# Optimization experiments

Hardware: AMD Instinct MI355X
Metric: run time of the kernel (lower is better)

## Reference

```python
import jax, jax.numpy as jnp
import numpy as np

EPS = 0.001  # additive floor applied after relu, as in the torch code


def setup_inputs() -> dict:
    key = jax.random.key(0)
    kA, kB, kW = jax.random.split(key, 3)
    M, N, C, H, W = 512, 64, 128, 8, 8
    A = jax.random.normal(kA, (M, C, H, W), dtype=jnp.float32)
    B = jax.random.normal(kB, (N, C, H, W), dtype=jnp.float32)
    Wg = jax.random.normal(kW, (C, C), dtype=jnp.float32) * 0.01  # Wg.data.normal_(0.0, 0.01)
    return {"A": A, "B": B, "Wg": Wg}


def reference(A, B, Wg):
    # Faithful vectorization of MIMOcom.get_source_dst_max(A, B, dir=True).
    # Torch loops i,j over HxW: B0 = B[:, i, j, :]; G = B0 @ Wg;
    # combination[m, n, p] = sum_c A[m, p, c] * G[n, c]; running max over (i, j).
    M, C, H, W = A.shape
    N = B.shape[0]
    P = H * W
    Af = jnp.transpose(A, (0, 2, 3, 1)).reshape(M, P, C)  # [M, P, C]
    Bf = jnp.transpose(B, (0, 2, 3, 1)).reshape(N, P, C)  # [N, Q, C]
    G = Bf @ Wg                                           # [N, Q, D]
    scores = jnp.einsum('mpd,nqd->mnpq', Af, G)           # [M, N, P, Q]
    comb_max = scores.max(axis=-1)                        # max over B positions q
    return jax.nn.relu(comb_max) + EPS                    # [M, N, P]
```

## Files before the change

kernel.cpp:

```cpp
#include <hip/hip_runtime.h>
#include <hip/hip_bf16.h>
#include <stdint.h>

typedef __attribute__((ext_vector_type(8))) short bf16x8;
typedef __attribute__((ext_vector_type(16))) float f32x16;
using bf16 = __hip_bfloat16;

static constexpr int Mdim = 512;
static constexpr int Ndim = 64;
static constexpr int Cdim = 128;
static constexpr int Pdim = 64;
static constexpr float EPS_ADD = 0.001f;

#define SB0 __builtin_amdgcn_sched_barrier(0)
#define WAITV(N) asm volatile("s_waitcnt vmcnt(" #N ")" ::: "memory")

__device__ __forceinline__ void gll16(const void* gsrc, void* ldst) {
    const __attribute__((address_space(1))) unsigned int* g =
        (const __attribute__((address_space(1))) unsigned int*)gsrc;
    __attribute__((address_space(3))) unsigned int* l =
        (__attribute__((address_space(3))) unsigned int*)(uintptr_t)ldst;
    __builtin_amdgcn_global_load_lds(g, l, 16, 0, 0);
}

__global__ void prep_kernel(const float* __restrict__ A, const float* __restrict__ B,
                            const float* __restrict__ Wg,
                            bf16* __restrict__ Afrag, bf16* __restrict__ Gfrag) {
    __shared__ float lds[128 * 65];
    const int t = threadIdx.x;

    if (blockIdx.x < 512) {
        const int m = blockIdx.x;
        const float* __restrict__ Am = A + (size_t)m * (Cdim * Pdim);
#pragma unroll
        for (int i = 0; i < 8; ++i) {
            int v = t + i * 256;
            int gidx = v * 4;
            int c = gidx >> 6, p = gidx & 63;
            float4 val = *reinterpret_cast<const float4*>(Am + gidx);
            float* dst = &lds[c * 65 + p];
            dst[0] = val.x; dst[1] = val.y; dst[2] = val.z; dst[3] = val.w;
        }
        __syncthreads();

        unsigned* __restrict__ dst32 = (unsigned*)(Afrag + (size_t)m * 8192);
#pragma unroll
        for (int i = 0; i < 16; ++i) {
            int pr = t + i * 256;
            int p = pr >> 6;
            int c = (pr & 63) << 1;
            float f0 = lds[c * 65 + p];
            float f1 = lds[(c + 1) * 65 + p];
            union { bf16 hh[2]; unsigned u; } pk;
            pk.hh[0] = __float2bfloat16(f0);
            pk.hh[1] = __float2bfloat16(f1);
            int h = p >> 5, l31 = p & 31;
            int ks = c >> 4, hi = (c >> 3) & 1, e = c & 7;
            dst32[h * 2048 + ks * 256 + hi * 128 + l31 * 4 + (e >> 1)] = pk.u;
        }
    } else {
        const int nb = blockIdx.x - 512;
        const int n  = nb >> 2;
        const int q0 = (nb & 3) * 16;
        const float* __restrict__ Bn = B + (size_t)n * (Cdim * Pdim);
#pragma unroll
        for (int i = 0; i < 8; ++i) {
            int v = t + i * 256;
            int gidx = v * 4;
            int c = gidx >> 6, q = gidx & 63;
            float4 val = *reinterpret_cast<const float4*>(Bn + gidx);
            float* dst = &lds[c * 65 + q];
            dst[0] = val.x; dst[1] = val.y; dst[2] = val.z; dst[3] = val.w;
        }
        __syncthreads();

        const int d  = t & 127;
        const int qb = q0 + (t >> 7) * 8;
        float acc[8] = {0.f, 0.f, 0.f, 0.f, 0.f, 0.f, 0.f, 0.f};
        for (int c = 0; c < 128; ++c) {
            float w = Wg[c * 128 + d];
#pragma unroll
            for (int qi = 0; qi < 8; ++qi)
                acc[qi] = fmaf(lds[c * 65 + qb + qi], w, acc[qi]);
        }
        bf16* __restrict__ gdst = Gfrag + (size_t)n * 8192;
        const int ks = d >> 4, hi = (d >> 3) & 1, e = d & 7;
#pragma unroll
        for (int qi = 0; qi < 8; ++qi) {
            int q = qb + qi;
            int qt = q >> 5, l31 = q & 31;
            gdst[qt * 4096 + ks * 512 + hi * 256 + l31 * 8 + e] = __float2bfloat16(acc[qi]);
        }
    }
}

__global__ __launch_bounds__(256, 3)
void gemm_max_kernel(const bf16* __restrict__ Afrag, const bf16* __restrict__ Gfrag,
                     float* __restrict__ out) {
    __shared__ bf16 sG[3][8192];
    const int tid  = threadIdx.x;
    const int lane = tid & 63;
    const int wv   = tid >> 6;
    const int mi = wv >> 1, h = wv & 1;
    const int l31 = lane & 31, hi = lane >> 5;
    const int mg = blockIdx.x & 127;
    const int bn = blockIdx.x >> 7;
    const int m0 = mg * 4 + mi * 2;

    bf16x8 a[2][8];
    {
#pragma unroll
        for (int u = 0; u < 2; ++u) {
            const bf16* Ap = Afrag + (size_t)(m0 + u) * 8192 + h * 4096 + lane * 8;
#pragma unroll
            for (int ks = 0; ks < 8; ++ks)
                a[u][ks] = *reinterpret_cast<const bf16x8*>(Ap + ks * 512);
        }
    }
    asm volatile("" ::: "memory");

    const char* Gsrc = (const char*)(Gfrag + (size_t)(bn * 8) * 8192);
    auto stageG = [&](int s) {
        char* dst = (char*)&sG[s % 3][0];
        const char* src = Gsrc + (size_t)s * 16384;
#pragma unroll
        for (int i = 0; i < 4; ++i) {
            int f = (i * 256 + tid) * 16;
            gll16(src + f, dst + f);
        }
    };
    stageG(0);
    stageG(1);

    const f32x16 z16 = {0.f,0.f,0.f,0.f,0.f,0.f,0.f,0.f,0.f,0.f,0.f,0.f,0.f,0.f,0.f,0.f};

    auto step = [&](int s) {
        const char* gb = (const char*)&sG[s % 3][0] + lane * 16;
        float r0, r1;
#pragma unroll
        for (int qt = 0; qt < 2; ++qt) {
            f32x16 acc0, acc1;
            __builtin_amdgcn_s_setprio(1);
#pragma unroll
            for (int ks = 0; ks < 8; ++ks) {
                bf16x8 gf = *reinterpret_cast<const bf16x8*>(gb + qt * 8192 + ks * 1024);
                acc0 = __builtin_amdgcn_mfma_f32_32x32x16_bf16(
                    gf, a[0][ks], ks == 0 ? z16 : acc0, 0, 0, 0);
                acc1 = __builtin_amdgcn_mfma_f32_32x32x16_bf16(
                    gf, a[1][ks], ks == 0 ? z16 : acc1, 0, 0, 0);
            }
            __builtin_amdgcn_s_setprio(0);
            float t0 = fmaxf(acc0[0], acc0[1]);
#pragma unroll
            for (int j = 2; j < 16; ++j) t0 = fmaxf(t0, acc0[j]);
            float t1 = fmaxf(acc1[0], acc1[1]);
#pragma unroll
            for (int j = 2; j < 16; ++j) t1 = fmaxf(t1, acc1[j]);
            if (qt == 0) { r0 = t0; r1 = t1; }
            else         { r0 = fmaxf(r0, t0); r1 = fmaxf(r1, t1); }
        }
        r0 = fmaxf(r0, __shfl_xor(r0, 32));
        r1 = fmaxf(r1, __shfl_xor(r1, 32));
        const int n = bn * 8 + s;
        if (hi == 0) {
            out[(size_t)m0 * 4096 + n * 64 + h * 32 + l31]       = fmaxf(r0, 0.f) + EPS_ADD;
            out[(size_t)(m0 + 1) * 4096 + n * 64 + h * 32 + l31] = fmaxf(r1, 0.f) + EPS_ADD;
        }
    };

    WAITV(4); __builtin_amdgcn_s_barrier(); SB0;
    stageG(2); step(0); SB0;

    WAITV(6); __builtin_amdgcn_s_barrier(); SB0;
    stageG(3); step(1); SB0;

    for (int s = 2; s <= 5; ++s) {
        WAITV(8); __builtin_amdgcn_s_barrier(); SB0;
        stageG(s + 2); step(s); SB0;
    }

    WAITV(8); __builtin_amdgcn_s_barrier(); SB0;
    step(6); SB0;

    WAITV(4); __builtin_amdgcn_s_barrier(); SB0;
    step(7);
}

extern "C" void kernel_launch(void* const* d_in, const int* in_sizes, int n_in,
                              void* d_out, int out_size, void* d_ws, size_t ws_size,
                              hipStream_t stream) {
    const float* A  = (const float*)d_in[0];
    const float* B  = (const float*)d_in[1];
    const float* Wg = (const float*)d_in[2];
    float* out = (float*)d_out;

    bf16* Afrag = (bf16*)d_ws;
    bf16* Gfrag = (bf16*)((char*)d_ws + (size_t)Mdim * Pdim * Cdim * sizeof(bf16));

    prep_kernel<<<768, 256, 0, stream>>>(A, B, Wg, Afrag, Gfrag);
    gemm_max_kernel<<<1024, 256, 0, stream>>>(Afrag, Gfrag, out);
}
```

Measured before the change: 45.70 us.

## Double per-wave M rows in gemm_max kernel and reorder G staging after compute

Each wave now keeps four A rows in registers instead of two, so every G fragment read from LDS feeds four MFMAs instead of two. This halves the grid to 512 blocks and lowers the launch-bounds occupancy target from 3 to 2 blocks to make room for the larger register footprint. The G-tile prefetch now issues after each step's compute, with adjusted vmcnt waits. Every lane also writes output, with the two half-waves covering different rows. The cost is fewer resident waves for hiding latency and less software-pipelining lead on G loads.

```diff
diff --git a/kernel.cpp b/kernel.cpp
--- a/kernel.cpp
+++ b/kernel.cpp
@@ -94,7 +94,7 @@
     }
 }
 
-__global__ __launch_bounds__(256, 3)
+__global__ __launch_bounds__(256, 2)
 void gemm_max_kernel(const bf16* __restrict__ Afrag, const bf16* __restrict__ Gfrag,
                      float* __restrict__ out) {
     __shared__ bf16 sG[3][8192];
@@ -103,19 +103,17 @@
     const int wv   = tid >> 6;
     const int mi = wv >> 1, h = wv & 1;
     const int l31 = lane & 31, hi = lane >> 5;
-    const int mg = blockIdx.x & 127;
-    const int bn = blockIdx.x >> 7;
-    const int m0 = mg * 4 + mi * 2;
-
-    bf16x8 a[2][8];
-    {
-#pragma unroll
-        for (int u = 0; u < 2; ++u) {
-            const bf16* Ap = Afrag + (size_t)(m0 + u) * 8192 + h * 4096 + lane * 8;
-#pragma unroll
-            for (int ks = 0; ks < 8; ++ks)
-                a[u][ks] = *reinterpret_cast<const bf16x8*>(Ap + ks * 512);
-        }
+    const int mg = blockIdx.x & 63;
+    const int bn = blockIdx.x >> 6;
+    const int m0 = mg * 8 + mi * 4;
+
+    bf16x8 a[4][8];
+#pragma unroll
+    for (int u = 0; u < 4; ++u) {
+        const bf16* Ap = Afrag + (size_t)(m0 + u) * 8192 + h * 4096 + lane * 8;
+#pragma unroll
+        for (int ks = 0; ks < 8; ++ks)
+            a[u][ks] = *reinterpret_cast<const bf16x8*>(Ap + ks * 512);
     }
     asm volatile("" ::: "memory");
 
@@ -136,53 +134,57 @@
 
     auto step = [&](int s) {
         const char* gb = (const char*)&sG[s % 3][0] + lane * 16;
-        float r0, r1;
+        float r0, r1, r2, r3;
 #pragma unroll
         for (int qt = 0; qt < 2; ++qt) {
-            f32x16 acc0, acc1;
+            f32x16 acc0, acc1, acc2, acc3;
             __builtin_amdgcn_s_setprio(1);
 #pragma unroll
             for (int ks = 0; ks < 8; ++ks) {
                 bf16x8 gf = *reinterpret_cast<const bf16x8*>(gb + qt * 8192 + ks * 1024);
-                acc0 = __builtin_amdgcn_mfma_f32_32x32x16_bf16(
-                    gf, a[0][ks], ks == 0 ? z16 : acc0, 0, 0, 0);
-                acc1 = __builtin_amdgcn_mfma_f32_32x32x16_bf16(
-                    gf, a[1][ks], ks == 0 ? z16 : acc1, 0, 0, 0);
+                acc0 = __builtin_amdgcn_mfma_f32_32x32x16_bf16(gf, a[0][ks], ks == 0 ? z16 : acc0, 0, 0, 0);
+                acc1 = __builtin_amdgcn_mfma_f32_32x32x16_bf16(gf, a[1][ks], ks == 0 ? z16 : acc1, 0, 0, 0);
+                acc2 = __builtin_amdgcn_mfma_f32_32x32x16_bf16(gf, a[2][ks], ks == 0 ? z16 : acc2, 0, 0, 0);
+                acc3 = __builtin_amdgcn_mfma_f32_32x32x16_bf16(gf, a[3][ks], ks == 0 ? z16 : acc3, 0, 0, 0);
             }
             __builtin_amdgcn_s_setprio(0);
             float t0 = fmaxf(acc0[0], acc0[1]);
-#pragma unroll
-            for (int j = 2; j < 16; ++j) t0 = fmaxf(t0, acc0[j]);
             float t1 = fmaxf(acc1[0], acc1[1]);
-#pragma unroll
-            for (int j = 2; j < 16; ++j) t1 = fmaxf(t1, acc1[j]);
-            if (qt == 0) { r0 = t0; r1 = t1; }
-            else         { r0 = fmaxf(r0, t0); r1 = fmaxf(r1, t1); }
+            float t2 = fmaxf(acc2[0], acc2[1]);
+            float t3 = fmaxf(acc3[0], acc3[1]);
+#pragma unroll
+            for (int j = 2; j < 16; ++j) {
+                t0 = fmaxf(t0, acc0[j]); t1 = fmaxf(t1, acc1[j]);
+                t2 = fmaxf(t2, acc2[j]); t3 = fmaxf(t3, acc3[j]);
+            }
+            if (qt == 0) { r0 = t0; r1 = t1; r2 = t2; r3 = t3; }
+            else { r0 = fmaxf(r0, t0); r1 = fmaxf(r1, t1);
+                   r2 = fmaxf(r2, t2); r3 = fmaxf(r3, t3); }
         }
         r0 = fmaxf(r0, __shfl_xor(r0, 32));
         r1 = fmaxf(r1, __shfl_xor(r1, 32));
+        r2 = fmaxf(r2, __shfl_xor(r2, 32));
+        r3 = fmaxf(r3, __shfl_xor(r3, 32));
         const int n = bn * 8 + s;
-        if (hi == 0) {
-            out[(size_t)m0 * 4096 + n * 64 + h * 32 + l31]       = fmaxf(r0, 0.f) + EPS_ADD;
-            out[(size_t)(m0 + 1) * 4096 + n * 64 + h * 32 + l31] = fmaxf(r1, 0.f) + EPS_ADD;
-        }
+        const float sa = hi ? r2 : r0;
+        const float sb = hi ? r3 : r1;
+        float* ob = out + (size_t)(m0 + hi * 2) * 4096 + n * 64 + h * 32 + l31;
+        ob[0]    = fmaxf(sa, 0.f) + EPS_ADD;
+        ob[4096] = fmaxf(sb, 0.f) + EPS_ADD;
     };
 
     WAITV(4); __builtin_amdgcn_s_barrier(); SB0;
-    stageG(2); step(0); SB0;
+    step(0); SB0; stageG(2); SB0;
+
+    for (int s = 1; s <= 5; ++s) {
+        WAITV(6); __builtin_amdgcn_s_barrier(); SB0;
+        step(s); SB0; stageG(s + 2); SB0;
+    }
 
     WAITV(6); __builtin_amdgcn_s_barrier(); SB0;
-    stageG(3); step(1); SB0;
-
-    for (int s = 2; s <= 5; ++s) {
-        WAITV(8); __builtin_amdgcn_s_barrier(); SB0;
-        stageG(s + 2); step(s); SB0;
-    }
-
-    WAITV(8); __builtin_amdgcn_s_barrier(); SB0;
     step(6); SB0;
 
-    WAITV(4); __builtin_amdgcn_s_barrier(); SB0;
+    WAITV(2); __builtin_amdgcn_s_barrier(); SB0;
     step(7);
 }
 
@@ -198,5 +200,5 @@
     bf16* Gfrag = (bf16*)((char*)d_ws + (size_t)Mdim * Pdim * Cdim * sizeof(bf16));
 
     prep_kernel<<<768, 256, 0, stream>>>(A, B, Wg, Afrag, Gfrag);
-    gemm_max_kernel<<<1024, 256, 0, stream>>>(Afrag, Gfrag, out);
-}
+    gemm_max_kernel<<<512, 256, 0, stream>>>(Afrag, Gfrag, out);
+}
```

Result: slower. 69.78 us (+52.7%).

## Double-buffer G fragments in registers and process 16 N per block

Applied to the files above, without the earlier changes.

Each block now covers 16 N values instead of 8, so the grid is halved and the A fragments held in registers are reused across more N. G fragments are prefetched from LDS into two register buffers so their loads overlap the MFMA chains, and the max reduction of one half is interleaved with the MFMAs of the other. Launch bounds drop to 2 blocks per SM to make room for the extra registers, and both halves now share one store. The price is lower occupancy and fewer blocks for a fixed 512x64 problem, which may hurt latency hiding and load balance across CUs.

```diff
diff --git a/kernel.cpp b/kernel.cpp
--- a/kernel.cpp
+++ b/kernel.cpp
@@ -13,7 +13,6 @@
 static constexpr float EPS_ADD = 0.001f;
 
 #define SB0 __builtin_amdgcn_sched_barrier(0)
-#define WAITV(N) asm volatile("s_waitcnt vmcnt(" #N ")" ::: "memory")
 
 __device__ __forceinline__ void gll16(const void* gsrc, void* ldst) {
     const __attribute__((address_space(1))) unsigned int* g =
@@ -94,7 +93,7 @@
     }
 }
 
-__global__ __launch_bounds__(256, 3)
+__global__ __launch_bounds__(256, 2)
 void gemm_max_kernel(const bf16* __restrict__ Afrag, const bf16* __restrict__ Gfrag,
                      float* __restrict__ out) {
     __shared__ bf16 sG[3][8192];
@@ -108,18 +107,16 @@
     const int m0 = mg * 4 + mi * 2;
 
     bf16x8 a[2][8];
-    {
-#pragma unroll
-        for (int u = 0; u < 2; ++u) {
-            const bf16* Ap = Afrag + (size_t)(m0 + u) * 8192 + h * 4096 + lane * 8;
-#pragma unroll
-            for (int ks = 0; ks < 8; ++ks)
-                a[u][ks] = *reinterpret_cast<const bf16x8*>(Ap + ks * 512);
-        }
+#pragma unroll
+    for (int u = 0; u < 2; ++u) {
+        const bf16* Ap = Afrag + (size_t)(m0 + u) * 8192 + h * 4096 + lane * 8;
+#pragma unroll
+        for (int ks = 0; ks < 8; ++ks)
+            a[u][ks] = *reinterpret_cast<const bf16x8*>(Ap + ks * 512);
     }
     asm volatile("" ::: "memory");
 
-    const char* Gsrc = (const char*)(Gfrag + (size_t)(bn * 8) * 8192);
+    const char* Gsrc = (const char*)(Gfrag + (size_t)(bn * 16) * 8192);
     auto stageG = [&](int s) {
         char* dst = (char*)&sG[s % 3][0];
         const char* src = Gsrc + (size_t)s * 16384;
@@ -133,57 +130,75 @@
     stageG(1);
 
     const f32x16 z16 = {0.f,0.f,0.f,0.f,0.f,0.f,0.f,0.f,0.f,0.f,0.f,0.f,0.f,0.f,0.f,0.f};
-
-    auto step = [&](int s) {
-        const char* gb = (const char*)&sG[s % 3][0] + lane * 16;
-        float r0, r1;
-#pragma unroll
-        for (int qt = 0; qt < 2; ++qt) {
-            f32x16 acc0, acc1;
-            __builtin_amdgcn_s_setprio(1);
-#pragma unroll
-            for (int ks = 0; ks < 8; ++ks) {
-                bf16x8 gf = *reinterpret_cast<const bf16x8*>(gb + qt * 8192 + ks * 1024);
-                acc0 = __builtin_amdgcn_mfma_f32_32x32x16_bf16(
-                    gf, a[0][ks], ks == 0 ? z16 : acc0, 0, 0, 0);
-                acc1 = __builtin_amdgcn_mfma_f32_32x32x16_bf16(
-                    gf, a[1][ks], ks == 0 ? z16 : acc1, 0, 0, 0);
-            }
-            __builtin_amdgcn_s_setprio(0);
-            float t0 = fmaxf(acc0[0], acc0[1]);
-#pragma unroll
-            for (int j = 2; j < 16; ++j) t0 = fmaxf(t0, acc0[j]);
-            float t1 = fmaxf(acc1[0], acc1[1]);
-#pragma unroll
-            for (int j = 2; j < 16; ++j) t1 = fmaxf(t1, acc1[j]);
-            if (qt == 0) { r0 = t0; r1 = t1; }
-            else         { r0 = fmaxf(r0, t0); r1 = fmaxf(r1, t1); }
-        }
-        r0 = fmaxf(r0, __shfl_xor(r0, 32));
-        r1 = fmaxf(r1, __shfl_xor(r1, 32));
-        const int n = bn * 8 + s;
-        if (hi == 0) {
-            out[(size_t)m0 * 4096 + n * 64 + h * 32 + l31]       = fmaxf(r0, 0.f) + EPS_ADD;
-            out[(size_t)(m0 + 1) * 4096 + n * 64 + h * 32 + l31] = fmaxf(r1, 0.f) + EPS_ADD;
-        }
-    };
-
-    WAITV(4); __builtin_amdgcn_s_barrier(); SB0;
-    stageG(2); step(0); SB0;
-
-    WAITV(6); __builtin_amdgcn_s_barrier(); SB0;
-    stageG(3); step(1); SB0;
-
-    for (int s = 2; s <= 5; ++s) {
-        WAITV(8); __builtin_amdgcn_s_barrier(); SB0;
-        stageG(s + 2); step(s); SB0;
+    f32x16 acc0, acc1;
+    bf16x8 gfA[8], gfB[8];
+
+    auto ldgf = [&](bf16x8 (&g)[8], const char* base) {
+#pragma unroll
+        for (int ks = 0; ks < 8; ++ks)
+            g[ks] = *reinterpret_cast<const bf16x8*>(base + ks * 1024);
+    };
+    auto mmcl = [&](const bf16x8 (&gf)[8]) {
+        __builtin_amdgcn_s_setprio(1);
+        acc0 = __builtin_amdgcn_mfma_f32_32x32x16_bf16(gf[0], a[0][0], z16, 0, 0, 0);
+        acc1 = __builtin_amdgcn_mfma_f32_32x32x16_bf16(gf[0], a[1][0], z16, 0, 0, 0);
+#pragma unroll
+        for (int ks = 1; ks < 8; ++ks) {
+            acc0 = __builtin_amdgcn_mfma_f32_32x32x16_bf16(gf[ks], a[0][ks], acc0, 0, 0, 0);
+            acc1 = __builtin_amdgcn_mfma_f32_32x32x16_bf16(gf[ks], a[1][ks], acc1, 0, 0, 0);
+        }
+        __builtin_amdgcn_s_setprio(0);
+    };
+    auto red16 = [&](const f32x16& v) -> float {
+        float x0 = fmaxf(v[0], v[1]),  x1 = fmaxf(v[2], v[3]);
+        float x2 = fmaxf(v[4], v[5]),  x3 = fmaxf(v[6], v[7]);
+        float x4 = fmaxf(v[8], v[9]),  x5 = fmaxf(v[10], v[11]);
+        float x6 = fmaxf(v[12], v[13]), x7 = fmaxf(v[14], v[15]);
+        x0 = fmaxf(x0, x1); x2 = fmaxf(x2, x3);
+        x4 = fmaxf(x4, x5); x6 = fmaxf(x6, x7);
+        return fmaxf(fmaxf(x0, x2), fmaxf(x4, x6));
+    };
+
+#define BODY(S, WV, DOSTAGE, DOPREF)                                          \
+    __builtin_amdgcn_s_barrier(); SB0;                                        \
+    if (DOSTAGE) stageG((S) + 2);                                             \
+    ldgf(gfB, (const char*)&sG[(S) % 3][0] + 8192 + lane * 16);               \
+    mmcl(gfA);                                                                \
+    asm volatile("s_waitcnt vmcnt(" #WV ")" ::: "memory"); SB0;               \
+    if (DOPREF) ldgf(gfA, (const char*)&sG[((S) + 1) % 3][0] + lane * 16);    \
+    {                                                                         \
+        float t0 = red16(acc0), t1 = red16(acc1);                             \
+        mmcl(gfB);                                                            \
+        t0 = fmaxf(t0, red16(acc0)); t1 = fmaxf(t1, red16(acc1));             \
+        t0 = fmaxf(t0, __shfl_xor(t0, 32));                                   \
+        t1 = fmaxf(t1, __shfl_xor(t1, 32));                                   \
+        const int n = bn * 16 + (S);                                          \
+        const float sv = hi ? t1 : t0;                                        \
+        out[(size_t)(m0 + hi) * 4096 + n * 64 + h * 32 + l31] =               \
+            fmaxf(sv, 0.f) + EPS_ADD;                                         \
     }
 
-    WAITV(8); __builtin_amdgcn_s_barrier(); SB0;
-    step(6); SB0;
-
-    WAITV(4); __builtin_amdgcn_s_barrier(); SB0;
-    step(7);
+    asm volatile("s_waitcnt vmcnt(4)" ::: "memory");
+    __builtin_amdgcn_s_barrier(); SB0;
+    ldgf(gfA, (const char*)&sG[0][0] + lane * 16);
+
+    BODY(0, 4, 1, 1)
+    BODY(1, 5, 1, 1)
+    BODY(2, 5, 1, 1)
+    BODY(3, 5, 1, 1)
+    BODY(4, 5, 1, 1)
+    BODY(5, 5, 1, 1)
+    BODY(6, 5, 1, 1)
+    BODY(7, 5, 1, 1)
+    BODY(8, 5, 1, 1)
+    BODY(9, 5, 1, 1)
+    BODY(10, 5, 1, 1)
+    BODY(11, 5, 1, 1)
+    BODY(12, 5, 1, 1)
+    BODY(13, 5, 1, 1)
+    BODY(14, 1, 0, 1)
+    BODY(15, 2, 0, 0)
+#undef BODY
 }
 
 extern "C" void kernel_launch(void* const* d_in, const int* in_sizes, int n_in,
@@ -198,5 +213,5 @@
     bf16* Gfrag = (bf16*)((char*)d_ws + (size_t)Mdim * Pdim * Cdim * sizeof(bf16));
 
     prep_kernel<<<768, 256, 0, stream>>>(A, B, Wg, Afrag, Gfrag);
-    gemm_max_kernel<<<1024, 256, 0, stream>>>(Afrag, Gfrag, out);
-}
+    gemm_max_kernel<<<512, 256, 0, stream>>>(Afrag, Gfrag, out);
+}
```

Result: slower. 47.48 us (+3.9%).
